# Performance work log

Measured on AMD Instinct MI355X. Metric: run time of the kernel, lower is better.

Reference implementation:

```python
import jax, jax.numpy as jnp
import numpy as np

B, S, H, E, V, T = 32, 128, 1024, 256, 16000, 48  # batch, src len, hidden(=2*dec_hid), emb, vocab, max_length
GRU_IN = H + H + E  # context + selective_read + embedding


def setup_inputs() -> dict:
    key = jax.random.key(0)
    ks = jax.random.split(key, 14)
    s = 0.02
    return {
        "input": jax.random.randint(ks[0], (B, S), 0, V),
        "hidden": jax.random.normal(ks[1], (B, H), jnp.float32),
        "encoder_outputs": jax.random.normal(ks[2], (B, S, H), jnp.float32),
        "max_length": T,
        "attn_W_w": jax.random.normal(ks[3], (H, H), jnp.float32) * s,
        "attn_W_b": jnp.zeros((H,), jnp.float32),
        "copy_W_w": jax.random.normal(ks[4], (H, H), jnp.float32) * s,
        "copy_W_b": jnp.zeros((H,), jnp.float32),
        "embedding": jax.random.normal(ks[5], (V, E), jnp.float32) * s,
        "W_ih": jax.random.normal(ks[6], (3 * H, GRU_IN), jnp.float32) * s,
        "W_hh": jax.random.normal(ks[7], (3 * H, H), jnp.float32) * s,
        "b_ih": jnp.zeros((3 * H,), jnp.float32),
        "b_hh": jnp.zeros((3 * H,), jnp.float32),
        "out_w": jax.random.normal(ks[8], (V, H), jnp.float32) * s,
        "out_b": jnp.zeros((V,), jnp.float32),
    }


def reference(input, hidden, encoder_outputs, max_length, attn_W_w, attn_W_b,
              copy_W_w, copy_W_b, embedding, W_ih, W_hh, b_ih, b_hh, out_w, out_b):
    Bd, Sd, Hd = encoder_outputs.shape
    Vd = out_w.shape[0]
    inp = input
    b_idx = jnp.arange(Bd)[:, None]
    NEG = -1000000.0
    # one_hot_input_seq.sum(dim=1)==0 -> tokens never present in the source; col 0 forced on
    counts = jnp.zeros((Bd, Vd + Sd), jnp.int32).at[b_idx, inp].add(1)
    missing = (counts == 0).at[:, 0].set(True)

    def gru_cell(x, h):
        gx = x @ W_ih.T + b_ih
        gh = h @ W_hh.T + b_hh
        r = jax.nn.sigmoid(gx[:, :Hd] + gh[:, :Hd])
        z = jax.nn.sigmoid(gx[:, Hd:2 * Hd] + gh[:, Hd:2 * Hd])
        n = jnp.tanh(gx[:, 2 * Hd:] + r * gh[:, 2 * Hd:])
        return (1.0 - z) * n + z * h

    def step(carry, _):
        sampled, h, sel_read = carry  # [B] int, [B,H], [B,H]
        th = h @ attn_W_w.T + attn_W_b
        attn = jax.nn.softmax(jnp.einsum('bsh,bh->bs', encoder_outputs, th), axis=1)
        context = jnp.einsum('bs,bsh->bh', attn, encoder_outputs)
        prev = jnp.where(sampled > Vd, 3, sampled)  # OOV -> UNK (note: strict >, as in source)
        emb = embedding[prev]
        x = jnp.concatenate([context, sel_read, emb], axis=1)  # [B, 2H+E]
        h_new = gru_cell(x, h)
        th2 = h_new @ copy_W_w.T + copy_W_b
        copy_seq = jnp.einsum('bsh,bh->bs', encoder_outputs, th2)  # [B,S]
        # bmm(copy_seq^T, one_hot_input_seq) == scatter-add into extended-vocab slots
        copy_scores = jnp.zeros((Bd, Vd + Sd), x.dtype).at[b_idx, inp].add(copy_seq)
        copy_scores = jnp.where(missing, NEG, copy_scores)
        gen = (h_new @ out_w.T + out_b).at[:, 0].set(NEG)
        probs = jax.nn.softmax(jnp.concatenate([gen, copy_scores], axis=1), axis=1)  # [B, 2V+S]
        final = jnp.concatenate([probs[:, :Vd], jnp.zeros((Bd, Sd), x.dtype)], axis=1) + probs[:, Vd:]
        log_probs = jnp.log(final + 1e-10)  # [B, V+S]
        new_sampled = jnp.argmax(log_probs, axis=1).astype(sampled.dtype)
        # one_hot gather at sampled token == positions where source token equals sample
        pos = (inp == new_sampled[:, None]).astype(x.dtype)
        selected = pos * copy_seq
        norm = selected / jnp.maximum(jnp.sum(jnp.abs(selected), axis=1, keepdims=True), 1e-12)
        sel_new = jnp.einsum('bs,bsh->bh', norm, encoder_outputs)
        return (new_sampled, h_new, sel_new), (log_probs, new_sampled)

    init_sampled = jnp.ones((Bd,), jnp.int32)
    init_sel = jnp.zeros((Bd, Hd), encoder_outputs.dtype)
    _, (lps, sids) = jax.lax.scan(step, (init_sampled, hidden, init_sel), None, length=max_length - 1)
    sos = jnp.full((1, Bd, Vd + Sd), 2.0, encoder_outputs.dtype)
    decoder_outputs = jnp.concatenate([sos, lps], axis=0)  # [T,B,V+S] (after source's permute)
    sampled_idxs = jnp.concatenate([init_sampled[None], sids], axis=0).T[:, :, None]  # [B,T,1]
    return decoder_outputs, sampled_idxs
```

## Files before the change

### kernel.cpp

```cpp
#include <hip/hip_runtime.h>

#define BB 32
#define SS 128
#define HH 1024
#define EE 256
#define VV 16000
#define TT 48
#define VSS (VV + SS)
#define GIN 2304
#define NEGV (-1000000.0f)

__device__ __forceinline__ float dot4(float4 a, float4 b) {
  return a.x * b.x + a.y * b.y + a.z * b.z + a.w * b.w;
}

__device__ __forceinline__ float wave_reduce_sum(float v) {
  for (int o = 32; o; o >>= 1) v += __shfl_down(v, o, 64);
  return v;
}

__global__ __launch_bounds__(256) void k_init(float* __restrict__ out,
                                              float* __restrict__ sel0,
                                              int* __restrict__ samp) {
  const int i = blockIdx.x * 256 + threadIdx.x;
  if (i < BB * VSS) out[i] = 2.0f;
  if (i < BB * HH) sel0[i] = 0.0f;
  if (i < BB) {
    samp[i] = 1;
    out[(size_t)TT * BB * VSS + (size_t)i * TT] = 1.0f;
  }
}

__global__ __launch_bounds__(256) void k_count(const int* __restrict__ inp,
                                               unsigned* __restrict__ mask) {
  const int i = blockIdx.x * 256 + threadIdx.x;
  if (i < BB * SS) {
    const int b = i / SS;
    atomicOr(&mask[inp[i]], 1u << b);
  }
}

__global__ __launch_bounds__(256) void k_th(const float* __restrict__ W,
                                            const float* __restrict__ bias,
                                            const float* __restrict__ hvec,
                                            float* __restrict__ thout) {
  __shared__ float s_h[HH];
  const int blk = blockIdx.x, tid = threadIdx.x;
  const int b = blk >> 3, bb = blk & 7;
  const int lane = tid & 63, wv = tid >> 6;
  for (int i = tid; i < HH; i += 256) s_h[i] = hvec[b * HH + i];
  __syncthreads();
  const float4* h4 = (const float4*)s_h;
  const int j0 = bb * 128 + wv * 32;
  for (int i = 0; i < 32; ++i) {
    const int j = j0 + i;
    const float4* wr = (const float4*)(W + (size_t)j * HH);
    float acc = 0.f;
#pragma unroll 4
    for (int k = lane; k < HH / 4; k += 64) acc += dot4(wr[k], h4[k]);
    acc = wave_reduce_sum(acc);
    if (lane == 0) thout[b * HH + j] = acc + bias[j];
  }
}

__global__ __launch_bounds__(512) void k_attn2(const float* __restrict__ th,
                                               const float* __restrict__ enc,
                                               float* __restrict__ ctx) {
  __shared__ float s_th[HH];
  __shared__ float s_sc[SS];
  __shared__ float s_red[512];
  const int b = blockIdx.x, tid = threadIdx.x;
  const int lane = tid & 63, wv = tid >> 6;
  for (int i = tid; i < HH; i += 512) s_th[i] = th[b * HH + i];
  __syncthreads();
  const float4* th4 = (const float4*)s_th;
  for (int s = wv; s < SS; s += 8) {
    const float4* er = (const float4*)(enc + ((size_t)b * SS + s) * HH);
    float acc = 0.f;
#pragma unroll 4
    for (int k = lane; k < HH / 4; k += 64) acc += dot4(er[k], th4[k]);
    acc = wave_reduce_sum(acc);
    if (lane == 0) s_sc[s] = acc;
  }
  __syncthreads();
  const float v = (tid < SS) ? s_sc[tid] : -3.4e38f;
  s_red[tid] = v;
  __syncthreads();
  for (int o = 256; o; o >>= 1) {
    if (tid < o) s_red[tid] = fmaxf(s_red[tid], s_red[tid + o]);
    __syncthreads();
  }
  const float m = s_red[0];
  __syncthreads();
  const float e = (tid < SS) ? expf(v - m) : 0.f;
  s_red[tid] = e;
  __syncthreads();
  for (int o = 256; o; o >>= 1) {
    if (tid < o) s_red[tid] += s_red[tid + o];
    __syncthreads();
  }
  const float den = s_red[0];
  __syncthreads();
  if (tid < SS) s_sc[tid] = e / den;
  __syncthreads();
  if (tid < 256) {
    const float4* eb = (const float4*)(enc + (size_t)b * SS * HH);
    float4 acc = make_float4(0.f, 0.f, 0.f, 0.f);
    for (int s = 0; s < SS; ++s) {
      const float a = s_sc[s];
      const float4 x = eb[s * (HH / 4) + tid];
      acc.x += a * x.x; acc.y += a * x.y; acc.z += a * x.z; acc.w += a * x.w;
    }
    ((float4*)(ctx + b * HH))[tid] = acc;
  }
}

__global__ __launch_bounds__(256) void k_gru3(const float* __restrict__ hc,
                                              const float* __restrict__ ctx,
                                              const float* __restrict__ sel,
                                              const float* __restrict__ embt,
                                              const int* __restrict__ samp,
                                              const float* __restrict__ Wih,
                                              const float* __restrict__ Whh,
                                              const float* __restrict__ bih,
                                              const float* __restrict__ bhh,
                                              float* __restrict__ gbuf) {
  __shared__ float s_x[32][130];
  const int blk = blockIdx.x, tid = threadIdx.x;
  const int lane = tid & 63, wv = tid >> 6;
  const int b = lane & 31, rp = lane >> 5;
  const int lb = tid >> 3, lg = tid & 7;
  const bool ih = blk < 384;
  const int base = (ih ? blk : blk - 384) * 8;
  const int row = base + 2 * wv + rp;
  float acc = 0.f;
  int ei = 0;
  if (ih) {
    const int p = samp[lb];
    ei = (p > VV) ? 3 : p;
    if (ei >= VV) ei = VV - 1;
  }
  const int NCH = ih ? 18 : 8;
  for (int ch = 0; ch < NCH; ++ch) {
    const float* src;
    if (ih) {
      if (ch < 8) src = ctx + lb * HH + ch * 128;
      else if (ch < 16) src = sel + lb * HH + (ch - 8) * 128;
      else src = embt + (size_t)ei * EE + (ch - 16) * 128;
    } else {
      src = hc + lb * HH + ch * 128;
    }
    float2* drow = (float2*)&s_x[lb][0];
#pragma unroll
    for (int m = 0; m < 4; ++m) {
      const int col = lg + m * 8;
      const float4 v4 = ((const float4*)src)[col];
      drow[2 * col] = make_float2(v4.x, v4.y);
      drow[2 * col + 1] = make_float2(v4.z, v4.w);
    }
    __syncthreads();
    const float4* wr = ih ? (const float4*)(Wih + (size_t)row * GIN + ch * 128)
                          : (const float4*)(Whh + (size_t)row * HH + ch * 128);
    const float2* xr = (const float2*)&s_x[b][0];
#pragma unroll 8
    for (int kc = 0; kc < 32; ++kc) {
      const float2 xa = xr[2 * kc], xb2 = xr[2 * kc + 1];
      acc += dot4(wr[kc], make_float4(xa.x, xa.y, xb2.x, xb2.y));
    }
    __syncthreads();
  }
  if (ih) {
    acc += bih[row];
    gbuf[(size_t)(row >> 10) * (BB * HH) + b * HH + (row & 1023)] = acc;
  } else {
    acc += bhh[row];
    gbuf[(size_t)(3 + (row >> 10)) * (BB * HH) + b * HH + (row & 1023)] = acc;
  }
}

__global__ __launch_bounds__(256) void k_grufin(const float* __restrict__ gbuf,
                                                const float* __restrict__ hc,
                                                float* __restrict__ hn) {
  const int gid = blockIdx.x * 256 + threadIdx.x;
  const int b = gid >> 10, j = gid & 1023;
  const int o = b * HH + j;
  const float gxr = gbuf[0 * (BB * HH) + o];
  const float gxz = gbuf[1 * (BB * HH) + o];
  const float gxn = gbuf[2 * (BB * HH) + o];
  const float ghr = gbuf[3 * (BB * HH) + o];
  const float ghz = gbuf[4 * (BB * HH) + o];
  const float ghn = gbuf[5 * (BB * HH) + o];
  const float rr = 1.f / (1.f + expf(-(gxr + ghr)));
  const float zz = 1.f / (1.f + expf(-(gxz + ghz)));
  const float nn = tanhf(gxn + rr * ghn);
  hn[o] = (1.f - zz) * nn + zz * hc[o];
}

__global__ __launch_bounds__(512) void k_copy2(const float* __restrict__ th2,
                                               const float* __restrict__ enc,
                                               const int* __restrict__ inp,
                                               float* __restrict__ cseq,
                                               float* __restrict__ cvals) {
  __shared__ float s_th[HH];
  __shared__ float s_sc[SS];
  const int b = blockIdx.x, tid = threadIdx.x;
  const int lane = tid & 63, wv = tid >> 6;
  for (int i = tid; i < HH; i += 512) s_th[i] = th2[b * HH + i];
  __syncthreads();
  const float4* th4 = (const float4*)s_th;
  for (int s = wv; s < SS; s += 8) {
    const float4* er = (const float4*)(enc + ((size_t)b * SS + s) * HH);
    float acc = 0.f;
#pragma unroll 4
    for (int k = lane; k < HH / 4; k += 64) acc += dot4(er[k], th4[k]);
    acc = wave_reduce_sum(acc);
    if (lane == 0) {
      s_sc[s] = acc;
      cseq[b * SS + s] = acc;
    }
  }
  for (int i = tid; i < VV; i += 512) cvals[(size_t)b * VV + i] = 0.f;
  __syncthreads();
  if (tid < SS) atomicAdd(&cvals[(size_t)b * VV + inp[b * SS + tid]], s_sc[tid]);
}

__global__ __launch_bounds__(256) void k_gen3(const float* __restrict__ hn,
                                              const float* __restrict__ Wo,
                                              const float* __restrict__ bo,
                                              float* __restrict__ gen) {
  __shared__ float s_h[32][130];
  const int blk = blockIdx.x, tid = threadIdx.x;
  const int lane = tid & 63, wv = tid >> 6;
  const int b = lane & 31, rp = lane >> 5;
  const int lb = tid >> 3, lg = tid & 7;
  const int v0 = blk * 16;
  const int va = v0 + 2 * wv + rp;
  const int vb = va + 8;
  float acc0 = 0.f, acc1 = 0.f;
  for (int ch = 0; ch < 8; ++ch) {
    const float* src = hn + lb * HH + ch * 128;
    float2* drow = (float2*)&s_h[lb][0];
#pragma unroll
    for (int m = 0; m < 4; ++m) {
      const int col = lg + m * 8;
      const float4 v4 = ((const float4*)src)[col];
      drow[2 * col] = make_float2(v4.x, v4.y);
      drow[2 * col + 1] = make_float2(v4.z, v4.w);
    }
    __syncthreads();
    const float4* wr0 = (const float4*)(Wo + (size_t)va * HH + ch * 128);
    const float4* wr1 = (const float4*)(Wo + (size_t)vb * HH + ch * 128);
    const float2* xr = (const float2*)&s_h[b][0];
#pragma unroll 8
    for (int kc = 0; kc < 32; ++kc) {
      const float2 xa = xr[2 * kc], xb2 = xr[2 * kc + 1];
      const float4 xv = make_float4(xa.x, xa.y, xb2.x, xb2.y);
      acc0 += dot4(wr0[kc], xv);
      acc1 += dot4(wr1[kc], xv);
    }
    __syncthreads();
  }
  gen[(size_t)b * VV + va] = acc0 + bo[va];
  gen[(size_t)b * VV + vb] = acc1 + bo[vb];
}

__global__ __launch_bounds__(1024) void k_out(const float* __restrict__ gen,
                                              const float* __restrict__ cvals,
                                              const unsigned* __restrict__ mask,
                                              const float* __restrict__ cseq,
                                              const int* __restrict__ inp,
                                              const float* __restrict__ enc,
                                              float* __restrict__ out,
                                              float* __restrict__ seln,
                                              int* __restrict__ samp,
                                              const int t) {
  __shared__ float s_red[1024];
  __shared__ int s_idx[1024];
  __shared__ float s_norm[SS];
  const int b = blockIdx.x, tid = threadIdx.x;
  const float* gb = gen + (size_t)b * VV;
  const float* cb = cvals + (size_t)b * VV;
  float m = -3.4e38f;
  for (int v = tid; v < VV; v += 1024) {
    const float gv = (v == 0) ? NEGV : gb[v];
    const float cv = (v == 0 || !((mask[v] >> b) & 1u)) ? NEGV : cb[v];
    m = fmaxf(m, fmaxf(gv, cv));
  }
  s_red[tid] = m;
  __syncthreads();
  for (int o = 512; o; o >>= 1) {
    if (tid < o) s_red[tid] = fmaxf(s_red[tid], s_red[tid + o]);
    __syncthreads();
  }
  m = s_red[0];
  __syncthreads();
  float sm = 0.f;
  for (int v = tid; v < VV; v += 1024) {
    const float gv = (v == 0) ? NEGV : gb[v];
    const float cv = (v == 0 || !((mask[v] >> b) & 1u)) ? NEGV : cb[v];
    sm += expf(gv - m) + expf(cv - m);
  }
  s_red[tid] = sm;
  __syncthreads();
  for (int o = 512; o; o >>= 1) {
    if (tid < o) s_red[tid] += s_red[tid + o];
    __syncthreads();
  }
  const float inv = 1.f / s_red[0];
  __syncthreads();
  float bv = -3.4e38f;
  int bi = VSS;
  float* ob = out + ((size_t)t * BB + b) * VSS;
  for (int v = tid; v < VV; v += 1024) {
    const float gv = (v == 0) ? NEGV : gb[v];
    const float cv = (v == 0 || !((mask[v] >> b) & 1u)) ? NEGV : cb[v];
    const float p = expf(gv - m) * inv + expf(cv - m) * inv;
    const float lp = logf(p + 1e-10f);
    ob[v] = lp;
    if (lp > bv) { bv = lp; bi = v; }
  }
  const float lpz = logf(1e-10f);
  for (int j = VV + tid; j < VSS; j += 1024) ob[j] = lpz;
  s_red[tid] = bv;
  s_idx[tid] = bi;
  __syncthreads();
  for (int o = 512; o; o >>= 1) {
    if (tid < o) {
      const float ov = s_red[tid + o];
      const int oi = s_idx[tid + o];
      if (ov > s_red[tid] || (ov == s_red[tid] && oi < s_idx[tid])) {
        s_red[tid] = ov;
        s_idx[tid] = oi;
      }
    }
    __syncthreads();
  }
  const int sp = s_idx[0];
  if (tid == 0) {
    samp[b] = sp;
    out[(size_t)TT * BB * VSS + (size_t)b * TT + t] = (float)sp;
  }
  __syncthreads();
  float sv = 0.f;
  if (tid < SS) sv = (inp[b * SS + tid] == sp) ? cseq[b * SS + tid] : 0.f;
  s_red[tid] = (tid < SS) ? fabsf(sv) : 0.f;
  __syncthreads();
  for (int o = 512; o; o >>= 1) {
    if (tid < o) s_red[tid] += s_red[tid + o];
    __syncthreads();
  }
  const float nf = 1.f / fmaxf(s_red[0], 1e-12f);
  __syncthreads();
  if (tid < SS) s_norm[tid] = sv * nf;
  __syncthreads();
  if (tid < 256) {
    const float4* eb = (const float4*)(enc + (size_t)b * SS * HH);
    float4 acc = make_float4(0.f, 0.f, 0.f, 0.f);
    for (int s = 0; s < SS; ++s) {
      const float a = s_norm[s];
      if (a != 0.f) {
        const float4 x = eb[s * (HH / 4) + tid];
        acc.x += a * x.x; acc.y += a * x.y; acc.z += a * x.z; acc.w += a * x.w;
      }
    }
    ((float4*)(seln + b * HH))[tid] = acc;
  }
}

extern "C" void kernel_launch(void* const* d_in, const int* in_sizes, int n_in,
                              void* d_out, int out_size, void* d_ws, size_t ws_size,
                              hipStream_t stream) {
  const int* inp = (const int*)d_in[0];
  const float* hidden = (const float*)d_in[1];
  const float* enc = (const float*)d_in[2];
  const float* Wa = (const float*)d_in[4];
  const float* ba = (const float*)d_in[5];
  const float* Wc = (const float*)d_in[6];
  const float* bc = (const float*)d_in[7];
  const float* emb = (const float*)d_in[8];
  const float* Wih = (const float*)d_in[9];
  const float* Whh = (const float*)d_in[10];
  const float* bih = (const float*)d_in[11];
  const float* bhh = (const float*)d_in[12];
  const float* Wo = (const float*)d_in[13];
  const float* bo = (const float*)d_in[14];
  float* out = (float*)d_out;

  float* ws = (float*)d_ws;
  float* hb0 = ws;
  float* hb1 = hb0 + BB * HH;
  float* sb0 = hb1 + BB * HH;
  float* sb1 = sb0 + BB * HH;
  float* ctx = sb1 + BB * HH;
  float* th = ctx + BB * HH;
  float* th2 = th + BB * HH;
  float* gbuf = th2 + BB * HH;
  float* cseq = gbuf + 6 * BB * HH;
  float* gen = cseq + BB * SS;
  float* cvals = gen + (size_t)BB * VV;
  unsigned* mask = (unsigned*)(cvals + (size_t)BB * VV);
  int* samp = (int*)(mask + VV);

  hipMemsetAsync(mask, 0, (size_t)VV * 4, stream);
  k_init<<<(BB * VSS + 255) / 256, 256, 0, stream>>>(out, sb0, samp);
  k_count<<<(BB * SS + 255) / 256, 256, 0, stream>>>(inp, mask);

  for (int t = 1; t < TT; ++t) {
    const float* hc = (t == 1) ? hidden : (((t - 1) & 1) ? hb0 : hb1);
    float* hw = (t & 1) ? hb0 : hb1;
    const float* sr = (t == 1) ? sb0 : (((t - 1) & 1) ? sb1 : sb0);
    float* sw = (t & 1) ? sb1 : sb0;

    k_th<<<BB * 8, 256, 0, stream>>>(Wa, ba, hc, th);
    k_attn2<<<BB, 512, 0, stream>>>(th, enc, ctx);
    k_gru3<<<768, 256, 0, stream>>>(hc, ctx, sr, emb, samp, Wih, Whh, bih, bhh,
                                    gbuf);
    k_grufin<<<BB * HH / 256, 256, 0, stream>>>(gbuf, hc, hw);
    k_th<<<BB * 8, 256, 0, stream>>>(Wc, bc, hw, th2);
    k_copy2<<<BB, 512, 0, stream>>>(th2, enc, inp, cseq, cvals);
    k_gen3<<<VV / 16, 256, 0, stream>>>(hw, Wo, bo, gen);
    k_out<<<BB, 1024, 0, stream>>>(gen, cvals, mask, cseq, inp, enc, out, sw, samp,
                                   t);
  }
}
```

Before: 11.04 ms.

## Fuse copy scoring into output kernel using shared-memory hash of source tokens

Removes the separate copy-score kernel, the dense per-batch cvals scatter buffer and the global presence mask. The output kernel now computes the copy scores itself and builds a 512-slot shared-memory open-addressing hash from source token to summed score. It then looks up each vocabulary entry in that hash and caches the gen and copy values in registers across the three softmax passes. This cuts one launch per step and roughly 2 MB of zero-fill and rereads per step. In exchange, the 32 output blocks now also do the 128x1024 dot products, and every vocab entry pays for hash probes.

Measured after the change: 10.47 ms. -5.1%, faster.

```diff
diff --git a/kernel.cpp b/kernel.cpp
--- a/kernel.cpp
+++ b/kernel.cpp
@@ -28,15 +28,6 @@
   if (i < BB) {
     samp[i] = 1;
     out[(size_t)TT * BB * VSS + (size_t)i * TT] = 1.0f;
-  }
-}
-
-__global__ __launch_bounds__(256) void k_count(const int* __restrict__ inp,
-                                               unsigned* __restrict__ mask) {
-  const int i = blockIdx.x * 256 + threadIdx.x;
-  if (i < BB * SS) {
-    const int b = i / SS;
-    atomicOr(&mask[inp[i]], 1u << b);
   }
 }
 
@@ -196,34 +187,6 @@
   hn[o] = (1.f - zz) * nn + zz * hc[o];
 }
 
-__global__ __launch_bounds__(512) void k_copy2(const float* __restrict__ th2,
-                                               const float* __restrict__ enc,
-                                               const int* __restrict__ inp,
-                                               float* __restrict__ cseq,
-                                               float* __restrict__ cvals) {
-  __shared__ float s_th[HH];
-  __shared__ float s_sc[SS];
-  const int b = blockIdx.x, tid = threadIdx.x;
-  const int lane = tid & 63, wv = tid >> 6;
-  for (int i = tid; i < HH; i += 512) s_th[i] = th2[b * HH + i];
-  __syncthreads();
-  const float4* th4 = (const float4*)s_th;
-  for (int s = wv; s < SS; s += 8) {
-    const float4* er = (const float4*)(enc + ((size_t)b * SS + s) * HH);
-    float acc = 0.f;
-#pragma unroll 4
-    for (int k = lane; k < HH / 4; k += 64) acc += dot4(er[k], th4[k]);
-    acc = wave_reduce_sum(acc);
-    if (lane == 0) {
-      s_sc[s] = acc;
-      cseq[b * SS + s] = acc;
-    }
-  }
-  for (int i = tid; i < VV; i += 512) cvals[(size_t)b * VV + i] = 0.f;
-  __syncthreads();
-  if (tid < SS) atomicAdd(&cvals[(size_t)b * VV + inp[b * SS + tid]], s_sc[tid]);
-}
-
 __global__ __launch_bounds__(256) void k_gen3(const float* __restrict__ hn,
                                               const float* __restrict__ Wo,
                                               const float* __restrict__ bo,
@@ -264,27 +227,68 @@
   gen[(size_t)b * VV + vb] = acc1 + bo[vb];
 }
 
-__global__ __launch_bounds__(1024) void k_out(const float* __restrict__ gen,
-                                              const float* __restrict__ cvals,
-                                              const unsigned* __restrict__ mask,
-                                              const float* __restrict__ cseq,
+__global__ __launch_bounds__(1024) void k_fin(const float* __restrict__ th2,
+                                              const float* __restrict__ enc,
                                               const int* __restrict__ inp,
-                                              const float* __restrict__ enc,
+                                              const float* __restrict__ gen,
                                               float* __restrict__ out,
                                               float* __restrict__ seln,
                                               int* __restrict__ samp,
                                               const int t) {
+  __shared__ float s_th[HH];
   __shared__ float s_red[1024];
   __shared__ int s_idx[1024];
+  __shared__ float s_sc[SS];
   __shared__ float s_norm[SS];
+  __shared__ int hkey[512];
+  __shared__ float hval[512];
   const int b = blockIdx.x, tid = threadIdx.x;
+  const int lane = tid & 63, wv = tid >> 6;
+  for (int i = tid; i < HH; i += 1024) s_th[i] = th2[b * HH + i];
+  if (tid < 512) { hkey[tid] = -1; hval[tid] = 0.f; }
+  __syncthreads();
+  const float4* th4 = (const float4*)s_th;
+  for (int s = wv; s < SS; s += 16) {
+    const float4* er = (const float4*)(enc + ((size_t)b * SS + s) * HH);
+    float acc = 0.f;
+#pragma unroll 4
+    for (int k = lane; k < HH / 4; k += 64) acc += dot4(er[k], th4[k]);
+    acc = wave_reduce_sum(acc);
+    if (lane == 0) s_sc[s] = acc;
+  }
+  __syncthreads();
+  if (tid < SS) {
+    const int tok = inp[b * SS + tid];
+    const float val = s_sc[tid];
+    unsigned h = ((unsigned)tok * 2654435761u) >> 23;
+    while (true) {
+      const int prev = atomicCAS(&hkey[h], -1, tok);
+      if (prev == -1 || prev == tok) { atomicAdd(&hval[h], val); break; }
+      h = (h + 1) & 511;
+    }
+  }
+  __syncthreads();
   const float* gb = gen + (size_t)b * VV;
-  const float* cb = cvals + (size_t)b * VV;
+  float gr[16], cr[16];
   float m = -3.4e38f;
-  for (int v = tid; v < VV; v += 1024) {
-    const float gv = (v == 0) ? NEGV : gb[v];
-    const float cv = (v == 0 || !((mask[v] >> b) & 1u)) ? NEGV : cb[v];
-    m = fmaxf(m, fmaxf(gv, cv));
+#pragma unroll
+  for (int k = 0; k < 16; ++k) {
+    const int v = tid + k * 1024;
+    if (v < VV) {
+      const float gv = (v == 0) ? NEGV : gb[v];
+      float cv = NEGV;
+      if (v != 0) {
+        unsigned h = ((unsigned)v * 2654435761u) >> 23;
+        while (true) {
+          const int kk = hkey[h];
+          if (kk == v) { cv = hval[h]; break; }
+          if (kk == -1) break;
+          h = (h + 1) & 511;
+        }
+      }
+      gr[k] = gv; cr[k] = cv;
+      m = fmaxf(m, fmaxf(gv, cv));
+    }
   }
   s_red[tid] = m;
   __syncthreads();
@@ -295,10 +299,10 @@
   m = s_red[0];
   __syncthreads();
   float sm = 0.f;
-  for (int v = tid; v < VV; v += 1024) {
-    const float gv = (v == 0) ? NEGV : gb[v];
-    const float cv = (v == 0 || !((mask[v] >> b) & 1u)) ? NEGV : cb[v];
-    sm += expf(gv - m) + expf(cv - m);
+#pragma unroll
+  for (int k = 0; k < 16; ++k) {
+    const int v = tid + k * 1024;
+    if (v < VV) sm += expf(gr[k] - m) + expf(cr[k] - m);
   }
   s_red[tid] = sm;
   __syncthreads();
@@ -311,13 +315,15 @@
   float bv = -3.4e38f;
   int bi = VSS;
   float* ob = out + ((size_t)t * BB + b) * VSS;
-  for (int v = tid; v < VV; v += 1024) {
-    const float gv = (v == 0) ? NEGV : gb[v];
-    const float cv = (v == 0 || !((mask[v] >> b) & 1u)) ? NEGV : cb[v];
-    const float p = expf(gv - m) * inv + expf(cv - m) * inv;
-    const float lp = logf(p + 1e-10f);
-    ob[v] = lp;
-    if (lp > bv) { bv = lp; bi = v; }
+#pragma unroll
+  for (int k = 0; k < 16; ++k) {
+    const int v = tid + k * 1024;
+    if (v < VV) {
+      const float p = expf(gr[k] - m) * inv + expf(cr[k] - m) * inv;
+      const float lp = logf(p + 1e-10f);
+      ob[v] = lp;
+      if (lp > bv) { bv = lp; bi = v; }
+    }
   }
   const float lpz = logf(1e-10f);
   for (int j = VV + tid; j < VSS; j += 1024) ob[j] = lpz;
@@ -342,7 +348,7 @@
   }
   __syncthreads();
   float sv = 0.f;
-  if (tid < SS) sv = (inp[b * SS + tid] == sp) ? cseq[b * SS + tid] : 0.f;
+  if (tid < SS) sv = (inp[b * SS + tid] == sp) ? s_sc[tid] : 0.f;
   s_red[tid] = (tid < SS) ? fabsf(sv) : 0.f;
   __syncthreads();
   for (int o = 512; o; o >>= 1) {
@@ -395,15 +401,10 @@
   float* th = ctx + BB * HH;
   float* th2 = th + BB * HH;
   float* gbuf = th2 + BB * HH;
-  float* cseq = gbuf + 6 * BB * HH;
-  float* gen = cseq + BB * SS;
-  float* cvals = gen + (size_t)BB * VV;
-  unsigned* mask = (unsigned*)(cvals + (size_t)BB * VV);
-  int* samp = (int*)(mask + VV);
-
-  hipMemsetAsync(mask, 0, (size_t)VV * 4, stream);
+  float* gen = gbuf + 6 * BB * HH;
+  int* samp = (int*)(gen + (size_t)BB * VV);
+
   k_init<<<(BB * VSS + 255) / 256, 256, 0, stream>>>(out, sb0, samp);
-  k_count<<<(BB * SS + 255) / 256, 256, 0, stream>>>(inp, mask);
 
   for (int t = 1; t < TT; ++t) {
     const float* hc = (t == 1) ? hidden : (((t - 1) & 1) ? hb0 : hb1);
@@ -417,9 +418,7 @@
                                     gbuf);
     k_grufin<<<BB * HH / 256, 256, 0, stream>>>(gbuf, hc, hw);
     k_th<<<BB * 8, 256, 0, stream>>>(Wc, bc, hw, th2);
-    k_copy2<<<BB, 512, 0, stream>>>(th2, enc, inp, cseq, cvals);
     k_gen3<<<VV / 16, 256, 0, stream>>>(hw, Wo, bo, gen);
-    k_out<<<BB, 1024, 0, stream>>>(gen, cvals, mask, cseq, inp, enc, out, sw, samp,
-                                   t);
-  }
-}
+    k_fin<<<BB, 1024, 0, stream>>>(th2, enc, inp, gen, out, sw, samp, t);
+  }
+}
```
